# Kernel optimization log

Measured on AMD Instinct MI355X. Metric: run time of the kernel, lower is better.

Reference implementation:

```python
import jax, jax.numpy as jnp
import numpy as np

N_NODES = 100000
N_EDGES = 1600000
D_IN = 256
D_OUT = 128


def setup_inputs() -> dict:
    key = jax.random.key(0)
    k1, k2, k3, k4, k5, k6 = jax.random.split(key, 6)
    x = jax.random.normal(k1, (N_NODES, D_IN), dtype=jnp.float32)
    src = jax.random.randint(k2, (N_EDGES,), 0, N_NODES, dtype=jnp.int64)
    dst = jnp.sort(jax.random.randint(k3, (N_EDGES,), 0, N_NODES, dtype=jnp.int64))
    w = jax.random.uniform(k4, (N_EDGES,), dtype=jnp.float32)
    # nn.Linear(input_size, output_size): weight [out, in], bias [out]
    bound = 1.0 / np.sqrt(D_IN)
    W = jax.random.uniform(k5, (D_OUT, D_IN), dtype=jnp.float32, minval=-bound, maxval=bound)
    b = jax.random.uniform(k6, (D_OUT,), dtype=jnp.float32, minval=-bound, maxval=bound)
    return {"x": x, "src": src, "dst": dst, "w": w, "W": W, "b": b}


def reference(x, src, dst, w, W, b):
    # h = linear(x)
    h = jnp.einsum("ni,oi->no", x, W) + b  # [N, D_OUT]
    # u_mul_e: message m_e = h[src_e] * w_e ; sum: out[v] = sum_{e: dst_e=v} m_e
    msgs = h[src] * w[:, None]  # [E, D_OUT]
    out = jax.ops.segment_sum(msgs, dst, num_segments=N_NODES)
    return out
```

## Files before the change

### kernel.cpp

```cpp
#include <hip/hip_runtime.h>

#define N_NODES 100000
#define N_EDGES 1600000
#define D_IN    256
#define D_OUT   128

typedef __attribute__((ext_vector_type(8))) short          bf16x8;
typedef __attribute__((ext_vector_type(8))) unsigned short ushort8;
typedef __attribute__((ext_vector_type(4))) float          f32x4;

__device__ inline unsigned short f2bf(float f) {
  union { float f; unsigned u; } v; v.f = f;
  unsigned r = v.u + 0x7fffu + ((v.u >> 16) & 1u);
  return (unsigned short)(r >> 16);
}
__device__ inline float bf2f(unsigned short u) {
  union { unsigned u; float f; } v; v.u = ((unsigned)u) << 16;
  return v.f;
}

__global__ __launch_bounds__(256) void gcn_prep_kernel(
    const float* __restrict__ W, unsigned short* __restrict__ Wp,
    const int* __restrict__ dst, int* __restrict__ row_ptr) {
  int gid = blockIdx.x * blockDim.x + threadIdx.x;
  if (gid < 4096) {
    int f = gid;
    int n = f >> 9, s = (f >> 6) & 7, lane = f & 63;
    int col = n * 16 + (lane & 15);
    int k0  = s * 32 + (lane >> 4) * 8;
#pragma unroll
    for (int j = 0; j < 8; ++j)
      Wp[f * 8 + j] = f2bf(W[col * D_IN + k0 + j]);
  } else {
    int v = gid - 4096;
    if (v > N_NODES) return;
    int lo = 0, hi = N_EDGES;
    while (lo < hi) {
      int mid = (lo + hi) >> 1;
      if (dst[mid] < v) lo = mid + 1; else hi = mid;
    }
    row_ptr[v] = lo;
  }
}

__global__ __launch_bounds__(512, 8) void gcn_linear_mfma_kernel(
    const float* __restrict__ x, const unsigned short* __restrict__ Wp,
    const float* __restrict__ b, unsigned short* __restrict__ h) {
  __shared__ unsigned short lW[16384];
  const int tid  = threadIdx.x;
  const int lane = tid & 63;
  const int wid  = tid >> 6;
  const int half = blockIdx.x & 1;
  const int r0   = (blockIdx.x >> 1) * 128 + wid * 16;

#pragma unroll
  for (int i = 0; i < 4; ++i) {
    int idx = i * 512 + tid;
    *(ushort8*)(&lW[idx * 8]) =
        *(const ushort8*)(Wp + ((size_t)(half * 2048 + idx)) * 8);
  }
  __syncthreads();

  int arow = r0 + (lane & 15);
  arow = arow < N_NODES ? arow : N_NODES - 1;
  const int kg = (lane >> 4) * 8;
  const float* xrow = x + (size_t)arow * D_IN + kg;

  f32x4 acc[4];
#pragma unroll
  for (int n = 0; n < 4; ++n) acc[n] = (f32x4){0.f, 0.f, 0.f, 0.f};

#pragma unroll
  for (int s = 0; s < 8; ++s) {
    float4 a0 = *(const float4*)(xrow + s * 32);
    float4 a1 = *(const float4*)(xrow + s * 32 + 4);
    bf16x8 af;
    af[0] = (short)f2bf(a0.x); af[1] = (short)f2bf(a0.y);
    af[2] = (short)f2bf(a0.z); af[3] = (short)f2bf(a0.w);
    af[4] = (short)f2bf(a1.x); af[5] = (short)f2bf(a1.y);
    af[6] = (short)f2bf(a1.z); af[7] = (short)f2bf(a1.w);
#pragma unroll
    for (int n = 0; n < 4; ++n) {
      bf16x8 bfrag = *(const bf16x8*)(&lW[(size_t)((n * 8 + s) * 64 + lane) * 8]);
      acc[n] = __builtin_amdgcn_mfma_f32_16x16x32_bf16(af, bfrag, acc[n], 0, 0, 0);
    }
  }

  __syncthreads();
  unsigned short* my = &lW[wid * 1024];
  const int col0 = lane & 15;
  const int q4   = (lane >> 4) * 4;
#pragma unroll
  for (int n = 0; n < 4; ++n) {
    const float bias = b[half * 64 + n * 16 + col0];
#pragma unroll
    for (int i = 0; i < 4; ++i)
      my[(q4 + i) * 64 + n * 16 + col0] = f2bf(acc[n][i] + bias);
  }
  __syncthreads();
#pragma unroll
  for (int j = 0; j < 2; ++j) {
    const int flat = j * 64 + lane;
    const int row  = flat >> 3;
    const int cin  = (flat & 7) * 8;
    if (r0 + row < N_NODES) {
      ushort8 v = *(const ushort8*)(&my[(size_t)flat * 8]);
      *(ushort8*)(&h[(size_t)(r0 + row) * D_OUT + half * 64 + cin]) = v;
    }
  }
}

__global__ __launch_bounds__(256) void gcn_agg_kernel(
    const unsigned short* __restrict__ h, const int* __restrict__ src,
    const float* __restrict__ w, const int* __restrict__ rp,
    float* __restrict__ out) {
  const int node = (blockIdx.x << 2) + (threadIdx.x >> 6);
  if (node >= N_NODES) return;
  const int lane = threadIdx.x & 63;
  const int g  = lane >> 4;
  const int dg = (lane & 15) << 3;

  const int s = rp[node], e = rp[node + 1];
  float acc[8];
#pragma unroll
  for (int j = 0; j < 8; ++j) acc[j] = 0.f;

  for (int base = s; base < e; base += 16) {
    const int i0 = base + (g << 2);
    if (i0 < e) {
      int   sv[4];
      float wv[4];
#pragma unroll
      for (int j = 0; j < 4; ++j) {
        int  i = i0 + j;
        bool valid = (i < e);
        int  ic = valid ? i : i0;
        sv[j] = src[ic];
        wv[j] = valid ? w[ic] : 0.f;
      }
      ushort8 hv[4];
#pragma unroll
      for (int j = 0; j < 4; ++j)
        hv[j] = *(const ushort8*)(h + (size_t)sv[j] * D_OUT + dg);
#pragma unroll
      for (int j = 0; j < 4; ++j)
#pragma unroll
        for (int k = 0; k < 8; ++k)
          acc[k] += bf2f(hv[j][k]) * wv[j];
    }
  }

#pragma unroll
  for (int j = 0; j < 8; ++j) acc[j] += __shfl_xor(acc[j], 16);
#pragma unroll
  for (int j = 0; j < 8; ++j) acc[j] += __shfl_xor(acc[j], 32);

  if (g == 0) {
    float4 o0 = {acc[0], acc[1], acc[2], acc[3]};
    float4 o1 = {acc[4], acc[5], acc[6], acc[7]};
    float* op = out + (size_t)node * D_OUT + dg;
    *(float4*)(op)     = o0;
    *(float4*)(op + 4) = o1;
  }
}

extern "C" void kernel_launch(void* const* d_in, const int* in_sizes, int n_in,
                              void* d_out, int out_size, void* d_ws, size_t ws_size,
                              hipStream_t stream) {
  const float* x   = (const float*)d_in[0];
  const int*   src = (const int*)d_in[1];
  const int*   dst = (const int*)d_in[2];
  const float* w   = (const float*)d_in[3];
  const float* W   = (const float*)d_in[4];
  const float* b   = (const float*)d_in[5];
  float* out = (float*)d_out;

  unsigned short* Wp = (unsigned short*)d_ws;
  unsigned short* h  = (unsigned short*)((char*)d_ws + 65536);
  int* row_ptr = (int*)((char*)d_ws + 65536 + (size_t)N_NODES * D_OUT * sizeof(unsigned short));

  gcn_prep_kernel<<<(4096 + N_NODES + 1 + 255) / 256, 256, 0, stream>>>(W, Wp, dst, row_ptr);
  gcn_linear_mfma_kernel<<<2 * ((N_NODES + 127) / 128), 512, 0, stream>>>(x, Wp, b, h);
  gcn_agg_kernel<<<N_NODES / 4, 256, 0, stream>>>(h, src, w, row_ptr, out);
}
```

Baseline: 110.6 us.

## Merge column halves into one 1024-thread block and drop LDS-staged output

New measurement: 112.6 us. About the same (+1.9%).

```diff
diff --git a/kernel.cpp b/kernel.cpp
--- a/kernel.cpp
+++ b/kernel.cpp
@@ -43,21 +43,20 @@
   }
 }
 
-__global__ __launch_bounds__(512, 8) void gcn_linear_mfma_kernel(
+__global__ __launch_bounds__(1024, 8) void gcn_linear_mfma_kernel(
     const float* __restrict__ x, const unsigned short* __restrict__ Wp,
     const float* __restrict__ b, unsigned short* __restrict__ h) {
-  __shared__ unsigned short lW[16384];
+  __shared__ unsigned short lW[32768];
   const int tid  = threadIdx.x;
   const int lane = tid & 63;
   const int wid  = tid >> 6;
-  const int half = blockIdx.x & 1;
-  const int r0   = (blockIdx.x >> 1) * 128 + wid * 16;
+  const int half = wid >> 3;
+  const int r0   = blockIdx.x * 128 + (wid & 7) * 16;
 
 #pragma unroll
   for (int i = 0; i < 4; ++i) {
-    int idx = i * 512 + tid;
-    *(ushort8*)(&lW[idx * 8]) =
-        *(const ushort8*)(Wp + ((size_t)(half * 2048 + idx)) * 8);
+    int idx = i * 1024 + tid;
+    *(ushort8*)(&lW[idx * 8]) = *(const ushort8*)(Wp + (size_t)idx * 8);
   }
   __syncthreads();
 
@@ -81,31 +80,23 @@
     af[6] = (short)f2bf(a1.z); af[7] = (short)f2bf(a1.w);
 #pragma unroll
     for (int n = 0; n < 4; ++n) {
-      bf16x8 bfrag = *(const bf16x8*)(&lW[(size_t)((n * 8 + s) * 64 + lane) * 8]);
+      const int n2 = half * 4 + n;
+      bf16x8 bfrag = *(const bf16x8*)(&lW[(size_t)((n2 * 8 + s) * 64 + lane) * 8]);
       acc[n] = __builtin_amdgcn_mfma_f32_16x16x32_bf16(af, bfrag, acc[n], 0, 0, 0);
     }
   }
 
-  __syncthreads();
-  unsigned short* my = &lW[wid * 1024];
   const int col0 = lane & 15;
   const int q4   = (lane >> 4) * 4;
 #pragma unroll
   for (int n = 0; n < 4; ++n) {
-    const float bias = b[half * 64 + n * 16 + col0];
+    const int col = half * 64 + n * 16 + col0;
+    const float bias = b[col];
 #pragma unroll
-    for (int i = 0; i < 4; ++i)
-      my[(q4 + i) * 64 + n * 16 + col0] = f2bf(acc[n][i] + bias);
-  }
-  __syncthreads();
-#pragma unroll
-  for (int j = 0; j < 2; ++j) {
-    const int flat = j * 64 + lane;
-    const int row  = flat >> 3;
-    const int cin  = (flat & 7) * 8;
-    if (r0 + row < N_NODES) {
-      ushort8 v = *(const ushort8*)(&my[(size_t)flat * 8]);
-      *(ushort8*)(&h[(size_t)(r0 + row) * D_OUT + half * 64 + cin]) = v;
+    for (int i = 0; i < 4; ++i) {
+      const int row = r0 + q4 + i;
+      if (row < N_NODES)
+        h[(size_t)row * D_OUT + col] = f2bf(acc[n][i] + bias);
     }
   }
 }
@@ -180,6 +171,6 @@
   int* row_ptr = (int*)((char*)d_ws + 65536 + (size_t)N_NODES * D_OUT * sizeof(unsigned short));
 
   gcn_prep_kernel<<<(4096 + N_NODES + 1 + 255) / 256, 256, 0, stream>>>(W, Wp, dst, row_ptr);
-  gcn_linear_mfma_kernel<<<2 * ((N_NODES + 127) / 128), 512, 0, stream>>>(x, Wp, b, h);
+  gcn_linear_mfma_kernel<<<(N_NODES + 127) / 128, 1024, 0, stream>>>(x, Wp, b, h);
   gcn_agg_kernel<<<N_NODES / 4, 256, 0, stream>>>(h, src, w, row_ptr, out);
 }
```
